# Kernel optimization log

Hardware: AMD Instinct MI355X
Metric: run time of the kernel (lower is better)

Reference implementation:

```python
import jax, jax.numpy as jnp
import numpy as np

B, T, D = 2, 2048, 2048
NH, HD = 16, 128
Q_LAT, KV_LAT = 1024, 512
EPS = 1e-6
THETA = 10000.0


def setup_inputs() -> dict:
    key = jax.random.key(0)
    ks = jax.random.split(key, 8)
    x = jax.random.normal(ks[0], (B, T, D), dtype=jnp.float32)
    # causal additive mask, broadcast over batch/heads
    neg = jnp.finfo(jnp.float32).min
    causal = jnp.where(jnp.tril(jnp.ones((T, T), dtype=bool)), 0.0, neg)
    attn_mask = causal[None, None, :, :].astype(jnp.float32)
    s = lambda fan_in: 1.0 / np.sqrt(fan_in)
    q_a_w = jax.random.normal(ks[1], (Q_LAT, D), dtype=jnp.float32) * s(D)
    q_b_w = jax.random.normal(ks[2], (NH * HD, Q_LAT), dtype=jnp.float32) * s(Q_LAT)
    kv_a_w = jax.random.normal(ks[3], (KV_LAT, D), dtype=jnp.float32) * s(D)
    k_b_w = jax.random.normal(ks[4], (NH * HD, KV_LAT), dtype=jnp.float32) * s(KV_LAT)
    v_b_w = jax.random.normal(ks[5], (NH * HD, KV_LAT), dtype=jnp.float32) * s(KV_LAT)
    o_w = jax.random.normal(ks[6], (D, NH * HD), dtype=jnp.float32) * s(NH * HD)
    q_norm_w = jnp.ones((HD,), dtype=jnp.float32)
    k_norm_w = jnp.ones((HD,), dtype=jnp.float32)
    return dict(x=x, attn_mask=attn_mask, q_a_w=q_a_w, q_b_w=q_b_w, kv_a_w=kv_a_w,
                k_b_w=k_b_w, v_b_w=v_b_w, o_w=o_w, q_norm_w=q_norm_w, k_norm_w=k_norm_w)


def _rms_norm(x, w):
    var = jnp.mean(jnp.square(x), axis=-1, keepdims=True)
    return x * jax.lax.rsqrt(var + EPS) * w


def _rope_cache(t, hd, dtype):
    inv_freq = 1.0 / (THETA ** (jnp.arange(0, hd, 2, dtype=jnp.float32) / hd))
    freqs = jnp.arange(t, dtype=jnp.float32)[:, None] * inv_freq[None, :]  # [t, hd/2]
    emb = jnp.concatenate([freqs, freqs], axis=-1)  # [t, hd]
    return jnp.cos(emb).astype(dtype), jnp.sin(emb).astype(dtype)


def _rotate_half(x):
    h = x.shape[-1] // 2
    return jnp.concatenate([-x[..., h:], x[..., :h]], axis=-1)


def reference(x, attn_mask, q_a_w, q_b_w, kv_a_w, k_b_w, v_b_w, o_w, q_norm_w, k_norm_w):
    b, t, d = x.shape
    # low-rank projections (torch Linear: y = x @ W.T)
    q = (x @ q_a_w.T) @ q_b_w.T          # [b, t, nh*hd]
    kv = x @ kv_a_w.T                     # [b, t, kv_lat]
    k = kv @ k_b_w.T
    v = kv @ v_b_w.T
    q = q.reshape(b, t, NH, HD).transpose(0, 2, 1, 3)  # [b, nh, t, hd]
    k = k.reshape(b, t, NH, HD).transpose(0, 2, 1, 3)
    v = v.reshape(b, t, NH, HD).transpose(0, 2, 1, 3)
    # QK-norm over head dim
    q = _rms_norm(q, q_norm_w)
    k = _rms_norm(k, k_norm_w)
    # RoPE
    cos, sin = _rope_cache(t, HD, x.dtype)  # [t, hd]
    cos = cos[None, None, :, :]
    sin = sin[None, None, :, :]
    q = q * cos + _rotate_half(q) * sin
    k = k * cos + _rotate_half(k) * sin
    # attention
    sd = 1.0 / np.sqrt(HD)
    attn = jnp.einsum('bhqd,bhkd->bhqk', q, k) * sd + attn_mask
    attn = jax.nn.softmax(attn, axis=-1)
    out = jnp.einsum('bhqk,bhkd->bhqd', attn, v)
    out = out.transpose(0, 2, 1, 3).reshape(b, t, NH * HD)
    return out @ o_w.T
```

## Files before the change

kernel.cpp:

```cpp
#include <hip/hip_runtime.h>
#include <hip/hip_fp16.h>

typedef _Float16 f16;
typedef _Float16 f16x4 __attribute__((ext_vector_type(4)));
typedef _Float16 f16x8 __attribute__((ext_vector_type(8)));
typedef float f32x4 __attribute__((ext_vector_type(4)));

#define BT 4096
#define DMODEL 2048

__device__ __forceinline__ void gld16(const f16* g, f16* l) {
    __builtin_amdgcn_global_load_lds((const __attribute__((address_space(1))) void*)g,
                                     (__attribute__((address_space(3))) void*)l, 16, 0, 0);
}

struct Cvt7 {
    const float* s[7];
    f16* d[7];
    int off4[8];
};
__global__ __launch_bounds__(256) void k_cvt7(Cvt7 c) {
    int i = blockIdx.x * 256 + threadIdx.x;
    if (i >= c.off4[7]) return;
    int seg = 0;
#pragma unroll
    for (int k = 1; k < 7; ++k) seg += (i >= c.off4[k]);
    int j = i - c.off4[seg];
    float4 v = ((const float4*)c.s[seg])[j];
    f16x4 h;
    h[0] = (f16)v.x; h[1] = (f16)v.y; h[2] = (f16)v.z; h[3] = (f16)v.w;
    ((f16x4*)c.d[seg])[j] = h;
}

template <int MODE, typename CT>
__global__ __launch_bounds__(512, 2) void k_gemm8(const f16* __restrict__ A,
                                                  const f16* __restrict__ B0,
                                                  const f16* __restrict__ B1,
                                                  CT* __restrict__ C0,
                                                  f16* __restrict__ C1,
                                                  int K, int nsplit, int ld0, int ld1) {
    __shared__ __align__(16) f16 lds[49152];
    const int tid = threadIdx.x;
    const int w = tid >> 6, l = tid & 63;
    const int wm = w >> 2, wn = w & 3;
    const int quad = l >> 4, ln = l & 15;
    const int m0 = blockIdx.y * 128, n0 = blockIdx.x * 256;

    const f16* Bp;
    if constexpr (MODE == 0) {
        Bp = B0 + (size_t)n0 * K;
    } else if constexpr (MODE == 1) {
        Bp = (n0 < nsplit) ? B0 + (size_t)n0 * K : B1 + (size_t)(n0 - nsplit) * K;
    } else {
        Bp = (n0 < 2048) ? B0 + (size_t)n0 * K : B1 + (size_t)(n0 - 2048) * K;
    }

    const f16* ag  = A + (size_t)(m0 + w * 16 + (l >> 2)) * K + (l & 3) * 8;
    const f16* bg0 = Bp + (size_t)(w * 16 + (l >> 2)) * K + (l & 3) * 8;
    const f16* bg1 = bg0 + (size_t)128 * K;
    f16* al = &lds[w * 512];
    f16* bl = &lds[4096 + w * 512];

#define STAGE8(buf_, kc_, t_)                          \
    {                                                  \
        const int off_ = ((buf_) * 2 + (kc_)) * 12288; \
        const int g_ = (t_) * 64 + (kc_) * 32;         \
        gld16(ag + g_, al + off_);                     \
        gld16(bg0 + g_, bl + off_);                    \
        gld16(bg1 + g_, bl + off_ + 4096);             \
    }

    f32x4 acc[4][4];
#pragma unroll
    for (int i = 0; i < 4; ++i)
#pragma unroll
        for (int j = 0; j < 4; ++j)
#pragma unroll
            for (int r = 0; r < 4; ++r) acc[i][j][r] = 0.f;

    const int nt = K >> 6;
    STAGE8(0, 0, 0);
    STAGE8(0, 1, 0);
    STAGE8(1, 0, 1);
    asm volatile("s_waitcnt vmcnt(3)" ::: "memory");
    __builtin_amdgcn_s_barrier();
    asm volatile("s_waitcnt lgkmcnt(0)" ::: "memory");

    for (int t = 0; t < nt; ++t) {
        const int buf = t & 1;
#pragma unroll
        for (int kc = 0; kc < 2; ++kc) {
            const f16* Ah = &lds[(buf * 2 + kc) * 12288];
            const f16* Bh = Ah + 4096;
            f16x8 a[4], b[4];
#pragma unroll
            for (int i = 0; i < 4; ++i)
                a[i] = *(const f16x8*)&Ah[(wm * 64 + i * 16 + ln) * 32 + quad * 8];
#pragma unroll
            for (int j = 0; j < 4; ++j)
                b[j] = *(const f16x8*)&Bh[(wn * 64 + j * 16 + ln) * 32 + quad * 8];
            if (kc == 0) {
                if (t + 1 < nt) STAGE8(buf ^ 1, 1, t + 1);
            } else {
                if (t + 2 < nt) STAGE8(buf, 0, t + 2);
            }
            __builtin_amdgcn_s_barrier();
            asm volatile("s_waitcnt lgkmcnt(0)" ::: "memory");
            __builtin_amdgcn_s_setprio(1);
#pragma unroll
            for (int i = 0; i < 4; ++i)
#pragma unroll
                for (int j = 0; j < 4; ++j)
                    acc[i][j] = __builtin_amdgcn_mfma_f32_16x16x32_f16(a[i], b[j], acc[i][j], 0, 0, 0);
            __builtin_amdgcn_s_setprio(0);
            if (kc == 1 && t + 1 < nt) {
                if (t + 2 < nt) asm volatile("s_waitcnt vmcnt(3)" ::: "memory");
                else            asm volatile("s_waitcnt vmcnt(0)" ::: "memory");
            }
            __builtin_amdgcn_s_barrier();
        }
    }
#undef STAGE8

    if constexpr (MODE == 2) {
        if (n0 >= 2048) {
            const int d0 = n0 - 2048;
            const int bb = m0 >> 11, tb = m0 & 2047;
#pragma unroll
            for (int i = 0; i < 4; ++i)
#pragma unroll
                for (int j = 0; j < 4; ++j) {
                    f16x4 v;
#pragma unroll
                    for (int r = 0; r < 4; ++r) v[r] = (f16)acc[i][j][r];
                    *(f16x4*)&C1[((size_t)(bb * 2048 + d0 + wn * 64 + j * 16 + ln)) * 2048 +
                                 tb + wm * 64 + i * 16 + quad * 4] = v;
                }
            return;
        }
    }

    CT* Cd; int ldc; int cb;
    if constexpr (MODE == 0) {
        Cd = C0; ldc = ld0; cb = n0;
    } else if constexpr (MODE == 1) {
        if (n0 < nsplit) { Cd = C0; ldc = ld0; cb = n0; }
        else             { Cd = (CT*)C1; ldc = ld1; cb = n0 - nsplit; }
    } else {
        Cd = C0; ldc = 2048; cb = n0;
    }

    const int p = (wm ? 16 : 0) + quad * 4;
    if constexpr (sizeof(CT) == 2) {
        f16* Cs = (f16*)lds;
#pragma unroll
        for (int i = 0; i < 4; ++i) {
            __syncthreads();
#pragma unroll
            for (int j = 0; j < 4; ++j)
#pragma unroll
                for (int r = 0; r < 4; ++r)
                    Cs[(p + r) * 264 + wn * 64 + j * 16 + ln] = (f16)acc[i][j][r];
            __syncthreads();
#pragma unroll
            for (int rr = 0; rr < 2; ++rr) {
                int idx = rr * 512 + tid;
                int row = idx >> 5, c8 = idx & 31;
                int rg = m0 + i * 16 + (row & 15) + ((row & 16) ? 64 : 0);
                *(f16x8*)&Cd[(size_t)rg * ldc + cb + c8 * 8] = *(const f16x8*)&Cs[row * 264 + c8 * 8];
            }
        }
    } else {
        float* Cs = (float*)lds;
#pragma unroll
        for (int i = 0; i < 4; ++i) {
            __syncthreads();
#pragma unroll
            for (int j = 0; j < 4; ++j)
#pragma unroll
                for (int r = 0; r < 4; ++r)
                    Cs[(p + r) * 260 + wn * 64 + j * 16 + ln] = acc[i][j][r];
            __syncthreads();
#pragma unroll
            for (int rr = 0; rr < 4; ++rr) {
                int idx = rr * 512 + tid;
                int row = idx >> 6, c4 = idx & 63;
                int rg = m0 + i * 16 + (row & 15) + ((row & 16) ? 64 : 0);
                *(float4*)&Cd[(size_t)rg * ldc + cb + c4 * 4] = *(const float4*)&Cs[row * 260 + c4 * 4];
            }
        }
    }
}

__global__ __launch_bounds__(256) void k_norm_rope(f16* __restrict__ q, f16* __restrict__ k,
                                                   const float* __restrict__ qw,
                                                   const float* __restrict__ kw) {
    const int gw = blockIdx.x * 4 + (threadIdx.x >> 6);
    const int l = threadIdx.x & 63;
    const int which = gw >> 16;
    const int rh = gw & 65535;
    const int row = rh >> 4, h = rh & 15;
    f16* p = which ? k : q;
    const float* wp = which ? kw : qw;
    const float scale = which ? 1.0f : 0.08838834764831843f;
    const size_t base = (size_t)row * DMODEL + h * 128;
    float xa = (float)p[base + l];
    float xb = (float)p[base + 64 + l];
    float ss = xa * xa + xb * xb;
#pragma unroll
    for (int off = 32; off > 0; off >>= 1) ss += __shfl_xor(ss, off);
    const float rms = rsqrtf(ss * (1.0f / 128.0f) + 1e-6f);
    const float na = xa * rms * wp[l];
    const float nb = xb * rms * wp[64 + l];
    const int t = row & 2047;
    const float freq = __expf((float)l * -0.1439115683121279f);
    const float ang = (float)t * freq;
    const float c = cosf(ang), s = sinf(ang);
    p[base + l]      = (f16)((na * c - nb * s) * scale);
    p[base + 64 + l] = (f16)((nb * c + na * s) * scale);
}

__global__ __launch_bounds__(256, 3) void k_flash(const f16* __restrict__ Q, const f16* __restrict__ K,
                                                  const f16* __restrict__ Vt, f16* __restrict__ O) {
    __shared__ f16 Kl[64 * 136];
    __shared__ f16 Vl[128 * 72];
    const int h = blockIdx.x, b = blockIdx.y, mt = 31 - blockIdx.z;
    const int tid = threadIdx.x, w = tid >> 6, l64 = tid & 63;
    const int quad = l64 >> 4, ln = l64 & 15;

    f16x8 qf[4];
    {
        const int tq = mt * 64 + w * 16 + ln;
        const f16* qp = Q + (size_t)(b * 2048 + tq) * DMODEL + h * 128 + quad * 8;
#pragma unroll
        for (int kc = 0; kc < 4; ++kc) qf[kc] = *(const f16x8*)(qp + kc * 32);
    }
    f32x4 oacc[8];
#pragma unroll
    for (int ot = 0; ot < 8; ++ot)
#pragma unroll
        for (int r = 0; r < 4; ++r) oacc[ot][r] = 0.f;
    float m_r = -INFINITY, l_r = 0.f;

    const f16* kbase = K + (size_t)(b * 2048) * DMODEL + h * 128;
    const f16* vbase = Vt + (size_t)(b * 2048 + h * 128) * 2048;

    f16x8 kr[4], vr[4];
#pragma unroll
    for (int c = 0; c < 4; ++c) {
        int idx = c * 256 + tid;
        kr[c] = *(const f16x8*)(kbase + (size_t)(idx >> 4) * DMODEL + (idx & 15) * 8);
        vr[c] = *(const f16x8*)(vbase + (size_t)(idx >> 3) * 2048 + (idx & 7) * 8);
    }

    for (int j = 0; j <= mt; ++j) {
        __syncthreads();
#pragma unroll
        for (int c = 0; c < 4; ++c) {
            int idx = c * 256 + tid;
            *(f16x8*)&Kl[(idx >> 4) * 136 + (idx & 15) * 8] = kr[c];
            *(f16x8*)&Vl[(idx >> 3) * 72 + (idx & 7) * 8] = vr[c];
        }
        __syncthreads();
        if (j < mt) {
#pragma unroll
            for (int c = 0; c < 4; ++c) {
                int idx = c * 256 + tid;
                kr[c] = *(const f16x8*)(kbase + (size_t)((j + 1) * 64 + (idx >> 4)) * DMODEL + (idx & 15) * 8);
                vr[c] = *(const f16x8*)(vbase + (size_t)(idx >> 3) * 2048 + (j + 1) * 64 + (idx & 7) * 8);
            }
        }
        f32x4 sacc[4];
#pragma unroll
        for (int nt = 0; nt < 4; ++nt)
#pragma unroll
            for (int r = 0; r < 4; ++r) sacc[nt][r] = 0.f;
#pragma unroll
        for (int nt = 0; nt < 4; ++nt)
#pragma unroll
            for (int kc = 0; kc < 4; ++kc) {
                f16x8 kf = *(const f16x8*)&Kl[(nt * 16 + ln) * 136 + kc * 32 + quad * 8];
                sacc[nt] = __builtin_amdgcn_mfma_f32_16x16x32_f16(kf, qf[kc], sacc[nt], 0, 0, 0);
            }
        if (j == mt) {
#pragma unroll
            for (int nt = 0; nt < 4; ++nt)
#pragma unroll
                for (int r = 0; r < 4; ++r)
                    if (nt * 16 + quad * 4 + r > w * 16 + ln) sacc[nt][r] = -INFINITY;
        }
        float mx = -INFINITY;
#pragma unroll
        for (int nt = 0; nt < 4; ++nt)
#pragma unroll
            for (int r = 0; r < 4; ++r) mx = fmaxf(mx, sacc[nt][r]);
        mx = fmaxf(mx, __shfl_xor(mx, 16));
        mx = fmaxf(mx, __shfl_xor(mx, 32));
        const bool grow = (mx > m_r + 8.f);
        const float mn = grow ? fmaxf(m_r, mx) : m_r;
        const float alpha = grow ? __expf(m_r - mn) : 1.f;
        m_r = mn;
        f16x4 pa[4];
        float s0 = 0.f;
#pragma unroll
        for (int nt = 0; nt < 4; ++nt)
#pragma unroll
            for (int r = 0; r < 4; ++r) {
                float pv = __expf(sacc[nt][r] - mn);
                s0 += pv;
                pa[nt][r] = (f16)pv;
            }
        s0 += __shfl_xor(s0, 16);
        s0 += __shfl_xor(s0, 32);
        l_r = l_r * alpha + s0;
        if (__ballot(grow)) {
            float ar[4];
#pragma unroll
            for (int r = 0; r < 4; ++r) ar[r] = __shfl(alpha, (l64 & 48) | (quad * 4 + r));
#pragma unroll
            for (int ot = 0; ot < 8; ++ot)
#pragma unroll
                for (int r = 0; r < 4; ++r) oacc[ot][r] *= ar[r];
        }
#pragma unroll
        for (int nt = 0; nt < 4; ++nt)
#pragma unroll
            for (int ot = 0; ot < 8; ++ot) {
                f16x4 vf = *(const f16x4*)&Vl[(ot * 16 + ln) * 72 + nt * 16 + quad * 4];
                oacc[ot] = __builtin_amdgcn_mfma_f32_16x16x16f16(pa[nt], vf, oacc[ot], 0, 0, 0);
            }
    }
    const float inv = 1.0f / l_r;
    float ivr[4];
#pragma unroll
    for (int r = 0; r < 4; ++r) ivr[r] = __shfl(inv, (l64 & 48) | (quad * 4 + r));
    __syncthreads();
#pragma unroll
    for (int ot = 0; ot < 8; ++ot)
#pragma unroll
        for (int r = 0; r < 4; ++r)
            Kl[(w * 16 + quad * 4 + r) * 136 + ot * 16 + ln] = (f16)(oacc[ot][r] * ivr[r]);
    __syncthreads();
#pragma unroll
    for (int c = 0; c < 4; ++c) {
        int idx = c * 256 + tid;
        int row = idx >> 4, col8 = (idx & 15) * 8;
        *(f16x8*)&O[(size_t)(b * 2048 + mt * 64 + row) * DMODEL + h * 128 + col8] =
            *(const f16x8*)&Kl[row * 136 + col8];
    }
}

extern "C" void kernel_launch(void* const* d_in, const int* in_sizes, int n_in,
                              void* d_out, int out_size, void* d_ws, size_t ws_size,
                              hipStream_t stream) {
    const float* x    = (const float*)d_in[0];
    const float* qaw  = (const float*)d_in[2];
    const float* qbw  = (const float*)d_in[3];
    const float* kvaw = (const float*)d_in[4];
    const float* kbw  = (const float*)d_in[5];
    const float* vbw  = (const float*)d_in[6];
    const float* ow   = (const float*)d_in[7];
    const float* qnw  = (const float*)d_in[8];
    const float* knw  = (const float*)d_in[9];
    float* out = (float*)d_out;

    char* p = (char*)d_ws;
    auto alloc = [&](size_t elems) { f16* r = (f16*)p; p += elems * sizeof(f16); return r; };
    f16* xb   = alloc((size_t)BT * 2048);
    f16* wo   = alloc((size_t)2048 * 2048);
    f16* wqa  = alloc((size_t)1024 * 2048);
    f16* wqb  = alloc((size_t)2048 * 1024);
    f16* wkva = alloc((size_t)512 * 2048);
    f16* wkb  = alloc((size_t)2048 * 512);
    f16* wvb  = alloc((size_t)2048 * 512);
    f16* qlat = alloc((size_t)BT * 1024);
    f16* kvb  = alloc((size_t)BT * 512);
    f16* qpre = alloc((size_t)BT * 2048);
    f16* kpre = alloc((size_t)BT * 2048);
    f16* vt   = xb;
    f16* attn = wqa;

    Cvt7 c;
    c.s[0] = x;    c.d[0] = xb;
    c.s[1] = qaw;  c.d[1] = wqa;
    c.s[2] = qbw;  c.d[2] = wqb;
    c.s[3] = kvaw; c.d[3] = wkva;
    c.s[4] = kbw;  c.d[4] = wkb;
    c.s[5] = vbw;  c.d[5] = wvb;
    c.s[6] = ow;   c.d[6] = wo;
    int sz4[7] = {BT * 2048 / 4, 1024 * 2048 / 4, 2048 * 1024 / 4, 512 * 2048 / 4,
                  2048 * 512 / 4, 2048 * 512 / 4, 2048 * 2048 / 4};
    c.off4[0] = 0;
    for (int i = 0; i < 7; ++i) c.off4[i + 1] = c.off4[i] + sz4[i];
    k_cvt7<<<(c.off4[7] + 255) / 256, 256, 0, stream>>>(c);

    k_gemm8<1, f16><<<dim3(1536 / 256, BT / 128), 512, 0, stream>>>(
        xb, wqa, wkva, qlat, kvb, 2048, 1024, 1024, 512);
    k_gemm8<0, f16><<<dim3(2048 / 256, BT / 128), 512, 0, stream>>>(
        qlat, wqb, nullptr, qpre, nullptr, 1024, 0, 2048, 0);
    k_gemm8<2, f16><<<dim3(4096 / 256, BT / 128), 512, 0, stream>>>(
        kvb, wkb, wvb, kpre, vt, 512, 0, 0, 0);
    k_norm_rope<<<32768, 256, 0, stream>>>(qpre, kpre, qnw, knw);
    k_flash<<<dim3(16, 2, 32), 256, 0, stream>>>(qpre, kpre, vt, attn);
    k_gemm8<0, float><<<dim3(2048 / 256, BT / 128), 512, 0, stream>>>(
        attn, wo, nullptr, out, nullptr, 2048, 0, 2048, 0);
}
```

Baseline: 390.6 us.

## Swizzle flash-attention LDS layout, raise occupancy, and remap workgroups for XCD locality

The flash kernel drops padded LDS rows and uses an XOR swizzle on the K, V and output staging buffers. This shrinks LDS use so more blocks fit per CU, and launch bounds are raised from 3 to 5 blocks. Both the GEMM and flash kernels remap the linear block index so consecutive chunks land on the same XCD, improving L2 reuse. The risks are register pressure at the higher occupancy, and index mapping that assumes fixed grid sizes (the GEMM assumes 32 row tiles).

Measured after the change: 482.0 us. 23.4% more time.

```diff
diff --git a/kernel.cpp b/kernel.cpp
--- a/kernel.cpp
+++ b/kernel.cpp
@@ -44,7 +44,11 @@
     const int w = tid >> 6, l = tid & 63;
     const int wm = w >> 2, wn = w & 3;
     const int quad = l >> 4, ln = l & 15;
-    const int m0 = blockIdx.y * 128, n0 = blockIdx.x * 256;
+    const int gx = gridDim.x;
+    const int lin = blockIdx.y * gx + blockIdx.x;
+    const int nwg = gx << 5;
+    const int chunk = (lin & 7) * (nwg >> 3) + (lin >> 3);
+    const int m0 = (chunk & 31) * 128, n0 = (chunk >> 5) * 256;
 
     const f16* Bp;
     if constexpr (MODE == 0) {
@@ -220,11 +224,13 @@
     p[base + 64 + l] = (f16)((nb * c + na * s) * scale);
 }
 
-__global__ __launch_bounds__(256, 3) void k_flash(const f16* __restrict__ Q, const f16* __restrict__ K,
+__global__ __launch_bounds__(256, 5) void k_flash(const f16* __restrict__ Q, const f16* __restrict__ K,
                                                   const f16* __restrict__ Vt, f16* __restrict__ O) {
-    __shared__ f16 Kl[64 * 136];
-    __shared__ f16 Vl[128 * 72];
-    const int h = blockIdx.x, b = blockIdx.y, mt = 31 - blockIdx.z;
+    __shared__ f16 Kl[64 * 128];
+    __shared__ f16 Vl[128 * 64];
+    const int lin = (blockIdx.z * 2 + blockIdx.y) * 16 + blockIdx.x;
+    const int chunk = (lin & 7) * 128 + (lin >> 3);
+    const int h = (chunk >> 5) & 15, b = chunk >> 9, mt = 31 - (chunk & 31);
     const int tid = threadIdx.x, w = tid >> 6, l64 = tid & 63;
     const int quad = l64 >> 4, ln = l64 & 15;
 
@@ -258,8 +264,9 @@
 #pragma unroll
         for (int c = 0; c < 4; ++c) {
             int idx = c * 256 + tid;
-            *(f16x8*)&Kl[(idx >> 4) * 136 + (idx & 15) * 8] = kr[c];
-            *(f16x8*)&Vl[(idx >> 3) * 72 + (idx & 7) * 8] = vr[c];
+            int krow = idx >> 4, vrow = idx >> 3;
+            *(f16x8*)&Kl[krow * 128 + (((idx & 15) ^ (krow & 7)) << 3)] = kr[c];
+            *(f16x8*)&Vl[vrow * 64 + (((idx & 7) ^ (vrow & 7)) << 3)] = vr[c];
         }
         __syncthreads();
         if (j < mt) {
@@ -279,7 +286,7 @@
         for (int nt = 0; nt < 4; ++nt)
 #pragma unroll
             for (int kc = 0; kc < 4; ++kc) {
-                f16x8 kf = *(const f16x8*)&Kl[(nt * 16 + ln) * 136 + kc * 32 + quad * 8];
+                f16x8 kf = *(const f16x8*)&Kl[(nt * 16 + ln) * 128 + (((kc * 4 + quad) ^ (ln & 7)) << 3)];
                 sacc[nt] = __builtin_amdgcn_mfma_f32_16x16x32_f16(kf, qf[kc], sacc[nt], 0, 0, 0);
             }
         if (j == mt) {
@@ -326,7 +333,7 @@
         for (int nt = 0; nt < 4; ++nt)
 #pragma unroll
             for (int ot = 0; ot < 8; ++ot) {
-                f16x4 vf = *(const f16x4*)&Vl[(ot * 16 + ln) * 72 + nt * 16 + quad * 4];
+                f16x4 vf = *(const f16x4*)&Vl[(ot * 16 + ln) * 64 + ((nt * 16 + quad * 4) ^ ((ln & 7) << 3))];
                 oacc[ot] = __builtin_amdgcn_mfma_f32_16x16x16f16(pa[nt], vf, oacc[ot], 0, 0, 0);
             }
     }
@@ -338,15 +345,17 @@
 #pragma unroll
     for (int ot = 0; ot < 8; ++ot)
 #pragma unroll
-        for (int r = 0; r < 4; ++r)
-            Kl[(w * 16 + quad * 4 + r) * 136 + ot * 16 + ln] = (f16)(oacc[ot][r] * ivr[r]);
+        for (int r = 0; r < 4; ++r) {
+            int row = w * 16 + quad * 4 + r;
+            Kl[row * 128 + ((ot * 16 + ln) ^ ((row & 7) << 3))] = (f16)(oacc[ot][r] * ivr[r]);
+        }
     __syncthreads();
 #pragma unroll
     for (int c = 0; c < 4; ++c) {
         int idx = c * 256 + tid;
-        int row = idx >> 4, col8 = (idx & 15) * 8;
-        *(f16x8*)&O[(size_t)(b * 2048 + mt * 64 + row) * DMODEL + h * 128 + col8] =
-            *(const f16x8*)&Kl[row * 136 + col8];
+        int row = idx >> 4, col8 = idx & 15;
+        *(f16x8*)&O[(size_t)(b * 2048 + mt * 64 + row) * DMODEL + h * 128 + col8 * 8] =
+            *(const f16x8*)&Kl[row * 128 + ((col8 ^ (row & 7)) << 3)];
     }
 }
 
```
